# Performance work log

Hardware: AMD Instinct MI355X
Metric: run time of the kernel (lower is better)

## Reference

```python
import jax, jax.numpy as jnp
import numpy as np

TOP_K = 32
TEMPERATURE = 1.0
PARAM_SCALE = 0.02


def setup_inputs() -> dict:
    key = jax.random.key(0)
    ks = jax.random.split(key, 7)
    B, S, D, F, P, R = 2, 1024, 1024, 4096, 256, 64
    x = jax.random.normal(ks[0], (B, S, D), dtype=jnp.float32)
    fc1_A = jax.random.normal(ks[1], (P, D, R), dtype=jnp.float32) * PARAM_SCALE
    fc1_B = jax.random.normal(ks[2], (P, R, F), dtype=jnp.float32) * PARAM_SCALE
    fc2_A = jax.random.normal(ks[3], (P, F, R), dtype=jnp.float32) * PARAM_SCALE
    fc2_B = jax.random.normal(ks[4], (P, R, D), dtype=jnp.float32) * PARAM_SCALE
    fc1_logits = jax.random.normal(ks[5], (P,), dtype=jnp.float32)
    fc2_logits = jax.random.normal(ks[6], (P,), dtype=jnp.float32)
    return {"x": x, "fc1_A": fc1_A, "fc1_B": fc1_B, "fc2_A": fc2_A,
            "fc2_B": fc2_B, "fc1_logits": fc1_logits, "fc2_logits": fc2_logits}


def _compose_weight(logits, A, B):
    """Top-k select primitives, softmax composition weights, weighted low-rank sum.

    A: (P, d_in, r), B: (P, r, d_out) -> W: (d_in, d_out)
    """
    vals, idx = jax.lax.top_k(logits, TOP_K)          # (K,), (K,)
    w = jax.nn.softmax(vals / TEMPERATURE)            # composition weights over selected
    A_sel = A[idx]                                    # (K, d_in, r) gather
    B_sel = B[idx]                                    # (K, r, d_out) gather
    return jnp.einsum('k,kir,kro->io', w, A_sel, B_sel)


def reference(x, fc1_A, fc1_B, fc2_A, fc2_B, fc1_logits, fc2_logits):
    W1 = _compose_weight(fc1_logits, fc1_A, fc1_B)    # (D, F)
    W2 = _compose_weight(fc2_logits, fc2_A, fc2_B)    # (F, D)
    h = jax.nn.gelu(jnp.einsum('bsd,df->bsf', x, W1))
    return jnp.einsum('bsf,fd->bsd', h, W2)
```

## Files before the change

kernel.cpp:

```cpp
#include <hip/hip_runtime.h>
#include <cstdint>
#include <cstddef>

typedef __attribute__((ext_vector_type(8))) short bhalf8;
typedef __attribute__((ext_vector_type(4))) float f32x4;

__device__ __forceinline__ unsigned short f2bf(float f){
    unsigned int u = __float_as_uint(f);
    u += 0x7fffu + ((u >> 16) & 1u);
    return (unsigned short)(u >> 16);
}

__device__ __forceinline__ float gelu_tanh(float x){
    const float c0 = 0.7978845608028654f;
    float x3 = x * x * x;
    float t = tanhf(c0 * (x + 0.044715f * x3));
    return 0.5f * x * (1.0f + t);
}

__device__ __forceinline__ void async_lds16(const unsigned short* g, unsigned short* l){
    __builtin_amdgcn_global_load_lds(
        (const __attribute__((address_space(1))) void*)g,
        (__attribute__((address_space(3))) void*)l, 16, 0, 0);
}

__global__ void topk_softmax_kernel(const float* __restrict__ lg1,
                                    const float* __restrict__ lg2,
                                    int* __restrict__ idx_out,
                                    float* __restrict__ w_out)
{
    const float* lg = (blockIdx.x == 0) ? lg1 : lg2;
    int*   idxo = idx_out + blockIdx.x * 32;
    float* wo   = w_out   + blockIdx.x * 32;
    const int lane = threadIdx.x;
    float v[4];
    #pragma unroll
    for (int j = 0; j < 4; ++j) v[j] = lg[lane * 4 + j];
    __shared__ float svals[32];
    for (int k = 0; k < 32; ++k){
        float bv = -1e30f; int bi = 0;
        #pragma unroll
        for (int j = 0; j < 4; ++j){
            if (v[j] > bv){ bv = v[j]; bi = lane * 4 + j; }
        }
        for (int off = 32; off > 0; off >>= 1){
            float ov = __shfl_down(bv, off);
            int   oi = __shfl_down(bi, off);
            if (ov > bv){ bv = ov; bi = oi; }
        }
        bi = __shfl(bi, 0);
        if (lane == 0){ svals[k] = bv; idxo[k] = bi; }
        if ((bi >> 2) == lane) v[bi & 3] = -1e30f;
    }
    float sv = svals[lane & 31];
    float e  = expf(sv - svals[0]);
    float s  = e;
    #pragma unroll
    for (int off = 16; off > 0; off >>= 1) s += __shfl_xor(s, off);
    if (lane < 32) wo[lane] = e / s;
}

__global__ void prep_gather_kernel(const float* __restrict__ x,  unsigned short* __restrict__ x16,
                                   const float* __restrict__ fc1A, unsigned short* __restrict__ Ag1,
                                   const float* __restrict__ fc1B, unsigned short* __restrict__ Bt1,
                                   const float* __restrict__ fc2A, unsigned short* __restrict__ Ag2,
                                   const float* __restrict__ fc2B, unsigned short* __restrict__ Bg2t,
                                   const int* __restrict__ idxb, const float* __restrict__ wb)
{
    __shared__ float tile[64][65];
    const int t = threadIdx.x;
    int b = blockIdx.x;

    if (b < 2048){
        int v = b * 256 + t;
        float4 xx = ((const float4*)x)[v];
        ushort4 o; o.x=f2bf(xx.x); o.y=f2bf(xx.y); o.z=f2bf(xx.z); o.w=f2bf(xx.w);
        ((ushort4*)x16)[v] = o;
        return;
    }
    b -= 2048;
    if (b < 10240){
        const float* src; unsigned short* dst; const int* idx; const float* w;
        int Drows, use_scale, v;
        if (b < 2048){ src=fc1A; dst=Ag1; idx=idxb;    w=wb;    Drows=1024; use_scale=1; v=b*256+t; }
        else         { src=fc2A; dst=Ag2; idx=idxb+32; w=wb+32; Drows=4096; use_scale=0; v=(b-2048)*256+t; }
        int c4 = v & 511;
        int d  = v >> 9;
        int k  = c4 >> 4;
        int r4 = c4 & 15;
        int p  = idx[k];
        float sc = use_scale ? w[k] : 1.0f;
        float4 xx = *((const float4*)(src + ((size_t)p * Drows + d) * 64) + r4);
        ushort4 o;
        o.x = f2bf(sc * xx.x); o.y = f2bf(sc * xx.y);
        o.z = f2bf(sc * xx.z); o.w = f2bf(sc * xx.w);
        *(ushort4*)(dst + (size_t)d * 2048 + k * 64 + r4 * 4) = o;
        return;
    }
    b -= 10240;
    const float* src; unsigned short* dst; const int* idx; const float* w;
    int Fcols, use_scale;
    if (b < 2048){ src=fc1B; dst=Bt1;  idx=idxb;    w=wb;    Fcols=4096; use_scale=0; }
    else         { src=fc2B; dst=Bg2t; idx=idxb+32; w=wb+32; Fcols=1024; use_scale=1; b -= 2048; }
    const int k  = b & 31;
    const int f0 = (b >> 5) * 64;
    const int p  = idx[k];
    const float sc = use_scale ? w[k] : 1.0f;
    const int cf = t & 15;
    const int r0 = t >> 4;
    #pragma unroll
    for (int pass = 0; pass < 4; ++pass){
        int r = r0 + pass * 16;
        float4 xx = *((const float4*)(src + ((size_t)p * 64 + r) * Fcols + f0) + cf);
        tile[r][cf * 4 + 0] = xx.x; tile[r][cf * 4 + 1] = xx.y;
        tile[r][cf * 4 + 2] = xx.z; tile[r][cf * 4 + 3] = xx.w;
    }
    __syncthreads();
    const int r4  = t & 15;
    const int fl0 = t >> 4;
    #pragma unroll
    for (int pass = 0; pass < 4; ++pass){
        int fl = fl0 + pass * 16;
        ushort4 o;
        o.x = f2bf(sc * tile[r4 * 4 + 0][fl]);
        o.y = f2bf(sc * tile[r4 * 4 + 1][fl]);
        o.z = f2bf(sc * tile[r4 * 4 + 2][fl]);
        o.w = f2bf(sc * tile[r4 * 4 + 3][fl]);
        *(ushort4*)(dst + (size_t)(f0 + fl) * 2048 + k * 64 + r4 * 4) = o;
    }
}

template<int EPI>
__device__ __forceinline__ void gemm_body(unsigned short* smem,
                                          const unsigned short* __restrict__ A,
                                          const unsigned short* __restrict__ Bt,
                                          void* __restrict__ Cout,
                                          int N, int K, int Kslice, int kbeg,
                                          int bm, int bn)
{
    unsigned short* sA0 = smem;
    unsigned short* sA1 = smem + 4096;
    unsigned short* sB0 = smem + 8192;
    unsigned short* sB1 = smem + 12288;
    const int t    = threadIdx.x;
    const int wave = t >> 6;
    const int lane = t & 63;
    const int wr   = (wave >> 1) * 64;
    const int wc   = (wave & 1) * 64;
    const int m16  = lane & 15;
    const int quad = lane >> 4;
    const int srow = t >> 2;
    const int scol = t & 3;

    f32x4 acc[4][4];
    const f32x4 z = {0.f, 0.f, 0.f, 0.f};
    #pragma unroll
    for (int i = 0; i < 4; ++i)
        #pragma unroll
        for (int j = 0; j < 4; ++j) acc[i][j] = z;

    const unsigned short* Arow = A  + (size_t)(bm + srow) * K + scol * 8 + kbeg;
    const unsigned short* Brow = Bt + (size_t)(bn + srow) * K + scol * 8 + kbeg;
    const size_t rstep = (size_t)64 * K;
    unsigned short* lA0 = sA0 + t * 8;
    unsigned short* lA1 = sA1 + t * 8;
    unsigned short* lB0 = sB0 + t * 8;
    unsigned short* lB1 = sB1 + t * 8;

    for (int k0 = 0; k0 < Kslice; k0 += 64){
        async_lds16(Arow + k0,              lA0);
        async_lds16(Arow + rstep + k0,      lA0 + 64 * 32);
        async_lds16(Arow + k0 + 32,         lA1);
        async_lds16(Arow + rstep + k0 + 32, lA1 + 64 * 32);
        async_lds16(Brow + k0,              lB0);
        async_lds16(Brow + rstep + k0,      lB0 + 64 * 32);
        async_lds16(Brow + k0 + 32,         lB1);
        async_lds16(Brow + rstep + k0 + 32, lB1 + 64 * 32);
        __syncthreads();

        bhalf8 af0[4], bf0[4], af1[4], bf1[4];
        #pragma unroll
        for (int i = 0; i < 4; ++i){
            af0[i] = *(const bhalf8*)(sA0 + (wr + i * 16 + m16) * 32 + quad * 8);
            af1[i] = *(const bhalf8*)(sA1 + (wr + i * 16 + m16) * 32 + quad * 8);
        }
        #pragma unroll
        for (int j = 0; j < 4; ++j){
            bf0[j] = *(const bhalf8*)(sB0 + (wc + j * 16 + m16) * 32 + quad * 8);
            bf1[j] = *(const bhalf8*)(sB1 + (wc + j * 16 + m16) * 32 + quad * 8);
        }

        #pragma unroll
        for (int i = 0; i < 4; ++i)
            #pragma unroll
            for (int j = 0; j < 4; ++j)
                acc[i][j] = __builtin_amdgcn_mfma_f32_16x16x32_bf16(af0[i], bf0[j], acc[i][j], 0, 0, 0);
        #pragma unroll
        for (int i = 0; i < 4; ++i)
            #pragma unroll
            for (int j = 0; j < 4; ++j)
                acc[i][j] = __builtin_amdgcn_mfma_f32_16x16x32_bf16(af1[i], bf1[j], acc[i][j], 0, 0, 0);
        __syncthreads();
    }

    #pragma unroll
    for (int i = 0; i < 4; ++i){
        #pragma unroll
        for (int j = 0; j < 4; ++j){
            #pragma unroll
            for (int r = 0; r < 4; ++r){
                int row = bm + wr + i * 16 + quad * 4 + r;
                int col = bn + wc + j * 16 + m16;
                float vv = acc[i][j][r];
                if (EPI == 1) vv = gelu_tanh(vv);
                if (EPI == 2) ((float*)Cout)[(size_t)row * N + col] = vv;
                else ((unsigned short*)Cout)[(size_t)row * N + col] = f2bf(vv);
            }
        }
    }
}

__device__ __forceinline__ int xcd_swz512(int id){ return (id & 7) * 64 + (id >> 3); }

__launch_bounds__(256, 2)
__global__ void gemm13_kernel(const unsigned short* __restrict__ A1,
                              const unsigned short* __restrict__ B1,
                              unsigned short* __restrict__ C1,
                              const unsigned short* __restrict__ A2,
                              const unsigned short* __restrict__ B2,
                              unsigned short* __restrict__ C2)
{
    __shared__ unsigned short smem[4 * 128 * 32];
    int id = xcd_swz512(blockIdx.x);
    if (id < 256){
        gemm_body<0>(smem, A1, B1, C1, 1024, 2048, 2048, 0,
                     (id >> 3) * 128, (id & 7) * 128);
    } else {
        id -= 256;
        gemm_body<0>(smem, A2, B2, C2, 4096, 2048, 2048, 0,
                     (id >> 5) * 128, (id & 31) * 128);
    }
}

__launch_bounds__(256, 2)
__global__ void gemm2_kernel(const unsigned short* __restrict__ A,
                             const unsigned short* __restrict__ Bt,
                             unsigned short* __restrict__ C)
{
    __shared__ unsigned short smem[4 * 128 * 32];
    int id = xcd_swz512(blockIdx.x);
    gemm_body<1>(smem, A, Bt, C, 4096, 1024, 1024, 0,
                 (id >> 5) * 128, (id & 31) * 128);
}

__launch_bounds__(256, 2)
__global__ void gemm4_kernel(const unsigned short* __restrict__ A,
                             const unsigned short* __restrict__ Bt,
                             float* __restrict__ part)
{
    __shared__ unsigned short smem[4 * 128 * 32];
    int id = xcd_swz512(blockIdx.x);
    int bz = id >> 7;
    int r  = id & 127;
    float* Cs = part + (size_t)bz * (2048 * 1024);
    gemm_body<2>(smem, A, Bt, Cs, 1024, 4096, 1024, bz * 1024,
                 (r >> 3) * 128, (r & 7) * 128);
}

__global__ void reduce4_kernel(const float4* __restrict__ p, float4* __restrict__ out)
{
    const int S = 524288;
    int v = blockIdx.x * 256 + threadIdx.x;
    float4 a = p[v], b = p[v + S], c = p[v + 2 * S], d = p[v + 3 * S];
    float4 r;
    r.x = (a.x + b.x) + (c.x + d.x);
    r.y = (a.y + b.y) + (c.y + d.y);
    r.z = (a.z + b.z) + (c.z + d.z);
    r.w = (a.w + b.w) + (c.w + d.w);
    out[v] = r;
}

extern "C" void kernel_launch(void* const* d_in, const int* in_sizes, int n_in,
                              void* d_out, int out_size, void* d_ws, size_t ws_size,
                              hipStream_t stream)
{
    const float* x    = (const float*)d_in[0];
    const float* fc1A = (const float*)d_in[1];
    const float* fc1B = (const float*)d_in[2];
    const float* fc2A = (const float*)d_in[3];
    const float* fc2B = (const float*)d_in[4];
    const float* lg1  = (const float*)d_in[5];
    const float* lg2  = (const float*)d_in[6];
    float* out = (float*)d_out;

    char* ws = (char*)d_ws;
    int*            idxb = (int*)(ws + 0);
    float*          wb   = (float*)(ws + 256);
    char* base = ws + 4096;
    unsigned short* x16  = (unsigned short*)(base);
    unsigned short* Ag1  = (unsigned short*)(base + (4ull  << 20));
    unsigned short* Bt1  = (unsigned short*)(base + (8ull  << 20));
    unsigned short* Ag2  = (unsigned short*)(base + (24ull << 20));
    unsigned short* Bg2t = (unsigned short*)(base + (40ull << 20));
    unsigned short* W1t  = (unsigned short*)(base + (44ull << 20));
    unsigned short* W2t  = (unsigned short*)(base + (52ull << 20));
    unsigned short* hbuf = (unsigned short*)(base + (60ull << 20));
    float*          part = (float*)(base + (76ull << 20));

    topk_softmax_kernel<<<dim3(2), dim3(64), 0, stream>>>(lg1, lg2, idxb, wb);

    prep_gather_kernel<<<dim3(14848), dim3(256), 0, stream>>>(
        x, x16, fc1A, Ag1, fc1B, Bt1, fc2A, Ag2, fc2B, Bg2t, idxb, wb);

    gemm13_kernel<<<dim3(512), dim3(256), 0, stream>>>(Bt1, Ag1, W1t, Bg2t, Ag2, W2t);

    gemm2_kernel<<<dim3(512), dim3(256), 0, stream>>>(x16, W1t, hbuf);

    gemm4_kernel<<<dim3(512), dim3(256), 0, stream>>>(hbuf, W2t, part);

    reduce4_kernel<<<dim3(2048), dim3(256), 0, stream>>>((const float4*)part, (float4*)out);
}
```

Measured before the change: 589.5 us.

## Double-buffer GEMM LDS tiles and use exp2/rcp GELU

Adds a second LDS stage to the shared GEMM body so the async global-to-LDS loads for the next K tile are issued before the MFMAs on the current tile, with one barrier per iteration instead of two. LDS per block doubles to 64 KB, which can still allow two blocks per CU under the existing launch bounds on this hardware. The tanh-form GELU is also rewritten as a sigmoid using hardware exp2 and reciprocal intrinsics to cut epilogue cost, at some loss of precision for large inputs.

```diff
diff --git a/kernel.cpp b/kernel.cpp
--- a/kernel.cpp
+++ b/kernel.cpp
@@ -12,10 +12,11 @@
 }
 
 __device__ __forceinline__ float gelu_tanh(float x){
-    const float c0 = 0.7978845608028654f;
-    float x3 = x * x * x;
-    float t = tanhf(c0 * (x + 0.044715f * x3));
-    return 0.5f * x * (1.0f + t);
+    const float c1 = 2.302584f;
+    float y  = x + 0.044715f * x * x * x;
+    float e  = __builtin_amdgcn_exp2f(c1 * y);
+    float r  = __builtin_amdgcn_rcpf(e + 1.0f);
+    return x - x * r;
 }
 
 __device__ __forceinline__ void async_lds16(const unsigned short* g, unsigned short* l){
@@ -138,10 +139,6 @@
                                           int N, int K, int Kslice, int kbeg,
                                           int bm, int bn)
 {
-    unsigned short* sA0 = smem;
-    unsigned short* sA1 = smem + 4096;
-    unsigned short* sB0 = smem + 8192;
-    unsigned short* sB1 = smem + 12288;
     const int t    = threadIdx.x;
     const int wave = t >> 6;
     const int lane = t & 63;
@@ -162,32 +159,39 @@
     const unsigned short* Arow = A  + (size_t)(bm + srow) * K + scol * 8 + kbeg;
     const unsigned short* Brow = Bt + (size_t)(bn + srow) * K + scol * 8 + kbeg;
     const size_t rstep = (size_t)64 * K;
-    unsigned short* lA0 = sA0 + t * 8;
-    unsigned short* lA1 = sA1 + t * 8;
-    unsigned short* lB0 = sB0 + t * 8;
-    unsigned short* lB1 = sB1 + t * 8;
-
-    for (int k0 = 0; k0 < Kslice; k0 += 64){
-        async_lds16(Arow + k0,              lA0);
-        async_lds16(Arow + rstep + k0,      lA0 + 64 * 32);
-        async_lds16(Arow + k0 + 32,         lA1);
-        async_lds16(Arow + rstep + k0 + 32, lA1 + 64 * 32);
-        async_lds16(Brow + k0,              lB0);
-        async_lds16(Brow + rstep + k0,      lB0 + 64 * 32);
-        async_lds16(Brow + k0 + 32,         lB1);
-        async_lds16(Brow + rstep + k0 + 32, lB1 + 64 * 32);
-        __syncthreads();
+
+    auto stage = [&](int slot, int k0){
+        unsigned short* s = smem + slot * 16384 + t * 8;
+        async_lds16(Arow + k0,              s);
+        async_lds16(Arow + rstep + k0,      s + 2048);
+        async_lds16(Arow + k0 + 32,         s + 4096);
+        async_lds16(Arow + rstep + k0 + 32, s + 6144);
+        async_lds16(Brow + k0,              s + 8192);
+        async_lds16(Brow + rstep + k0,      s + 10240);
+        async_lds16(Brow + k0 + 32,         s + 12288);
+        async_lds16(Brow + rstep + k0 + 32, s + 14336);
+    };
+
+    const int nIter = Kslice >> 6;
+
+    stage(0, 0);
+    asm volatile("s_waitcnt vmcnt(0)" ::: "memory");
+    __builtin_amdgcn_s_barrier();
+
+    for (int it = 0; it < nIter; ++it){
+        unsigned short* sb = smem + (it & 1) * 16384;
+        if (it + 1 < nIter) stage((it + 1) & 1, (it + 1) * 64);
 
         bhalf8 af0[4], bf0[4], af1[4], bf1[4];
         #pragma unroll
         for (int i = 0; i < 4; ++i){
-            af0[i] = *(const bhalf8*)(sA0 + (wr + i * 16 + m16) * 32 + quad * 8);
-            af1[i] = *(const bhalf8*)(sA1 + (wr + i * 16 + m16) * 32 + quad * 8);
+            af0[i] = *(const bhalf8*)(sb +         (wr + i * 16 + m16) * 32 + quad * 8);
+            af1[i] = *(const bhalf8*)(sb + 4096  + (wr + i * 16 + m16) * 32 + quad * 8);
         }
         #pragma unroll
         for (int j = 0; j < 4; ++j){
-            bf0[j] = *(const bhalf8*)(sB0 + (wc + j * 16 + m16) * 32 + quad * 8);
-            bf1[j] = *(const bhalf8*)(sB1 + (wc + j * 16 + m16) * 32 + quad * 8);
+            bf0[j] = *(const bhalf8*)(sb + 8192  + (wc + j * 16 + m16) * 32 + quad * 8);
+            bf1[j] = *(const bhalf8*)(sb + 12288 + (wc + j * 16 + m16) * 32 + quad * 8);
         }
 
         #pragma unroll
@@ -200,7 +204,11 @@
             #pragma unroll
             for (int j = 0; j < 4; ++j)
                 acc[i][j] = __builtin_amdgcn_mfma_f32_16x16x32_bf16(af1[i], bf1[j], acc[i][j], 0, 0, 0);
-        __syncthreads();
+
+        if (it + 1 < nIter){
+            asm volatile("s_waitcnt vmcnt(0) lgkmcnt(0)" ::: "memory");
+            __builtin_amdgcn_s_barrier();
+        }
     }
 
     #pragma unroll
@@ -230,7 +238,7 @@
                               const unsigned short* __restrict__ B2,
                               unsigned short* __restrict__ C2)
 {
-    __shared__ unsigned short smem[4 * 128 * 32];
+    __shared__ unsigned short smem[2 * 16384];
     int id = xcd_swz512(blockIdx.x);
     if (id < 256){
         gemm_body<0>(smem, A1, B1, C1, 1024, 2048, 2048, 0,
@@ -247,7 +255,7 @@
                              const unsigned short* __restrict__ Bt,
                              unsigned short* __restrict__ C)
 {
-    __shared__ unsigned short smem[4 * 128 * 32];
+    __shared__ unsigned short smem[2 * 16384];
     int id = xcd_swz512(blockIdx.x);
     gemm_body<1>(smem, A, Bt, C, 4096, 1024, 1024, 0,
                  (id >> 5) * 128, (id & 31) * 128);
@@ -258,7 +266,7 @@
                              const unsigned short* __restrict__ Bt,
                              float* __restrict__ part)
 {
-    __shared__ unsigned short smem[4 * 128 * 32];
+    __shared__ unsigned short smem[2 * 16384];
     int id = xcd_swz512(blockIdx.x);
     int bz = id >> 7;
     int r  = id & 127;
```

Result: no change. 578.8 us (-1.8%).
